# Performance work log

Measured on AMD Instinct MI355X. Metric: run time of the kernel, lower is better.

The kernel has to match this reference:

```python
import jax, jax.numpy as jnp
import numpy as np

Q_HEADS, KV_HEADS, D_K, D_V = 16, 4, 128, 128
GROUPS = Q_HEADS // KV_HEADS


def setup_inputs() -> dict:
    key = jax.random.key(0)
    ks = jax.random.split(key, 7)
    b, s, d = 2, 2048, 2048
    scale = 1.0 / np.sqrt(d).astype(np.float32)
    return {
        "Q": jax.random.normal(ks[0], (b, s, d), jnp.float32),
        "K": jax.random.normal(ks[1], (b, s, d), jnp.float32),
        "V": jax.random.normal(ks[2], (b, s, d), jnp.float32),
        "Wq": jax.random.normal(ks[3], (d, D_K * Q_HEADS), jnp.float32) * scale,
        "Wk": jax.random.normal(ks[4], (d, D_K * KV_HEADS), jnp.float32) * scale,
        "Wv": jax.random.normal(ks[5], (d, D_V * KV_HEADS), jnp.float32) * scale,
        "Wo": jax.random.normal(ks[6], (D_V * KV_HEADS, d), jnp.float32) * scale,
    }


def reference(Q, K, V, Wq, Wk, Wv, Wo):
    b, lq, _ = Q.shape
    lk = K.shape[1]
    # projections -> (b, heads, len, d)
    q = (Q @ Wq).reshape(b, lq, Q_HEADS, D_K).transpose(0, 2, 1, 3)
    k = (K @ Wk).reshape(b, lk, KV_HEADS, D_K).transpose(0, 2, 1, 3)
    v = (V @ Wv).reshape(b, lk, KV_HEADS, D_V).transpose(0, 2, 1, 3)
    # GQA quirk: scores summed over group dim g before softmax
    qr = q.reshape(b, GROUPS, KV_HEADS, lq, D_K)
    scores = jnp.einsum('bghqd,bhkd->bhqk', qr, k) / jnp.asarray(D_K ** 0.5, q.dtype)
    causal = jnp.tril(jnp.ones((lq, lk), bool))
    scores = jnp.where(causal[None, None], scores, jnp.asarray(-1e9, scores.dtype))
    attn = jax.nn.softmax(scores, axis=-1)  # (b, kv_heads, lq, lk)
    out = jnp.einsum('bhqk,bhkd->bhqd', attn, v)  # (b, kv_heads, lq, d_v)
    out = out.transpose(0, 2, 1, 3).reshape(b, lq, KV_HEADS * D_V)
    return out @ Wo
```

## Files before the change

### kernel.cpp

```cpp
#include <hip/hip_runtime.h>
#include <hip/hip_bf16.h>

typedef __attribute__((ext_vector_type(8))) short short8;
typedef __attribute__((ext_vector_type(4))) float f32x4;

#define MFMA16 __builtin_amdgcn_mfma_f32_16x16x32_bf16

__device__ inline unsigned short f2bf(float f) {
  __hip_bfloat16 h = __float2bfloat16(f);
  unsigned short u;
  __builtin_memcpy(&u, &h, 2);
  return u;
}

__device__ inline float bf2f(unsigned short u) {
  unsigned int x = ((unsigned int)u) << 16;
  float f;
  __builtin_memcpy(&f, &x, 4);
  return f;
}

__device__ inline void storeC(unsigned short* p, float v) { *p = f2bf(v); }
__device__ inline void storeC(float* p, float v) { *p = v; }

__device__ inline void gload16(const void* g, void* l) {
  __builtin_amdgcn_global_load_lds(
      (const __attribute__((address_space(1))) unsigned int*)g,
      (__attribute__((address_space(3))) unsigned int*)l,
      16, 0, 0);
}

__global__ __launch_bounds__(256)
void prep_all(const float* __restrict__ Wq, const float* __restrict__ Wk,
              const float* __restrict__ Wv, const float* __restrict__ Wo,
              unsigned short* __restrict__ Wt, unsigned short* __restrict__ WoT) {
  __shared__ float t[64][65];
  const int bid = blockIdx.x;
  const int tid = threadIdx.x;
  if (bid < 256) {
    const int n0 = (bid & 7) * 64, d0 = (bid >> 3) * 64;
#pragma unroll
    for (int it = 0; it < 16; ++it) {
      const int idx = it * 256 + tid;
      const int dd = idx >> 6, nn = idx & 63;
      const float* p = Wq + (size_t)(d0 + dd) * 2048 + n0 + nn;
      t[dd][nn] = p[0] + p[512] + p[1024] + p[1536];
    }
    __syncthreads();
#pragma unroll
    for (int it = 0; it < 16; ++it) {
      const int idx = it * 256 + tid;
      const int nn = idx >> 6, dd = idx & 63;
      Wt[(size_t)(n0 + nn) * 2048 + d0 + dd] = f2bf(t[dd][nn]);
    }
    return;
  }
  const float* src;
  unsigned short* dst;
  int R, C, c0, r0;
  if (bid < 768) {
    const int b = bid - 256;
    const int z = b >> 8;
    const int bb = b & 255;
    src = z ? Wv : Wk;
    dst = Wt + (z ? 2097152 : 1048576);
    R = 2048; C = 512;
    c0 = (bb & 7) * 64; r0 = (bb >> 3) * 64;
  } else {
    const int b = bid - 768;
    src = Wo; dst = WoT;
    R = 512; C = 2048;
    c0 = (b & 31) * 64; r0 = (b >> 5) * 64;
  }
#pragma unroll
  for (int it = 0; it < 16; ++it) {
    const int idx = it * 256 + tid;
    const int r = idx >> 6, c = idx & 63;
    t[r][c] = src[(size_t)(r0 + r) * C + c0 + c];
  }
  __syncthreads();
#pragma unroll
  for (int it = 0; it < 16; ++it) {
    const int idx = it * 256 + tid;
    const int rr = idx >> 6, cc = idx & 63;
    dst[(size_t)(c0 + rr) * R + r0 + cc] = f2bf(t[cc][rr]);
  }
}

template <bool AF32, typename CT, int KS>
__global__ __launch_bounds__(256)
void gemm_bt(const void* A0, const void* A1, const void* A2,
             const unsigned short* __restrict__ Bt, CT* __restrict__ C,
             int K, int N, size_t sB, size_t sC) {
  __shared__ unsigned short As[AF32 ? 1 : 2][128 * 64];
  __shared__ unsigned short Bs[2][128 * 64];

  const int tid = threadIdx.x;
  const int lane = tid & 63;
  const int wv = tid >> 6;
  const int wm = (wv >> 1) << 6;
  const int wn = (wv & 1) << 6;
  const int l15 = lane & 15;
  const int l4 = lane >> 4;
  const int lsw = (l15 & 7) << 4;

  const int nwg = gridDim.x;
  const int bid = blockIdx.x;
  const int job = (bid & 7) * (nwg >> 3) + (bid >> 3);
  const int ntile = N >> 7;
  const int per_ks = nwg / KS;
  const int ks = (KS > 1) ? (job / per_ks) : 0;
  const int jj = job - ks * per_ks;
  const int z = jj / (32 * ntile);
  const int rem = jj - z * 32 * ntile;
  const int m0 = (rem / ntile) << 7;
  const int n0 = (rem % ntile) << 7;
  const int kbeg = ks * (K / KS);
  const int kend = kbeg + K / KS;

  const void* Az = (z == 0) ? A0 : (z == 1) ? A1 : A2;
  const unsigned short* Ab = (const unsigned short*)Az;
  const float* Af = (const float*)Az;
  const unsigned short* Bz = Bt + sB * (size_t)z;

  const f32x4 zero = {0.f, 0.f, 0.f, 0.f};
  f32x4 acc[4][4];
#pragma unroll
  for (int i = 0; i < 4; ++i)
#pragma unroll
    for (int j = 0; j < 4; ++j) acc[i][j] = zero;

  const int srow = tid >> 3;
  const int scol = (tid & 7) << 3;
  const int scolsw = scol ^ ((srow & 7) << 3);

  float4 ar[8];

  auto issueB = [&](int buf, int k0) {
#pragma unroll
    for (int s = 0; s < 4; ++s) {
      const unsigned short* bsrc =
          Bz + (size_t)(n0 + srow + s * 32) * K + k0 + scolsw;
      gload16(bsrc, (char*)&Bs[buf][0] + tid * 16 + s * 4096);
    }
  };
  auto issueA16 = [&](int buf, int k0) {
#pragma unroll
    for (int s = 0; s < 4; ++s) {
      const unsigned short* asrc =
          Ab + (size_t)(m0 + srow + s * 32) * K + k0 + scolsw;
      gload16(asrc, (char*)&As[buf][0] + tid * 16 + s * 4096);
    }
  };
  auto loadA = [&](int k0) {
#pragma unroll
    for (int s = 0; s < 4; ++s) {
      const float* asrc = Af + (size_t)(m0 + srow + s * 32) * K + k0 + scol;
      ar[2 * s] = *(const float4*)(asrc);
      ar[2 * s + 1] = *(const float4*)(asrc + 4);
    }
  };
  auto writeA = [&]() {
#pragma unroll
    for (int s = 0; s < 4; ++s) {
      short8 o;
      o[0] = (short)f2bf(ar[2 * s].x); o[1] = (short)f2bf(ar[2 * s].y);
      o[2] = (short)f2bf(ar[2 * s].z); o[3] = (short)f2bf(ar[2 * s].w);
      o[4] = (short)f2bf(ar[2 * s + 1].x); o[5] = (short)f2bf(ar[2 * s + 1].y);
      o[6] = (short)f2bf(ar[2 * s + 1].z); o[7] = (short)f2bf(ar[2 * s + 1].w);
      *(short8*)((char*)&As[0][0] + (srow + s * 32) * 128 + scolsw * 2) = o;
    }
  };

  if constexpr (AF32) loadA(kbeg); else issueA16(0, kbeg);
  issueB(0, kbeg);

  int cur = 0;
  for (int k0 = kbeg; k0 < kend; k0 += 64) {
    const bool more = (k0 + 64 < kend);
    asm volatile("s_waitcnt vmcnt(0)" ::: "memory");
    if constexpr (AF32) {
      writeA();
      if (more) { issueB(cur ^ 1, k0 + 64); loadA(k0 + 64); }
      asm volatile("s_waitcnt lgkmcnt(0)" ::: "memory");
    } else {
      if (more) { issueA16(cur ^ 1, k0 + 64); issueB(cur ^ 1, k0 + 64); }
    }
    __builtin_amdgcn_s_barrier();
    const unsigned short* as = AF32 ? &As[0][0] : &As[cur][0];
#pragma unroll
    for (int kk = 0; kk < 2; ++kk) {
      const int kb = (kk * 64 + (l4 << 4)) ^ lsw;
      short8 a[4], b[4];
#pragma unroll
      for (int i = 0; i < 4; ++i)
        a[i] = *(const short8*)((const char*)as + (wm + i * 16 + l15) * 128 + kb);
#pragma unroll
      for (int j = 0; j < 4; ++j)
        b[j] = *(const short8*)((const char*)&Bs[cur][0] +
                                (wn + j * 16 + l15) * 128 + kb);
#pragma unroll
      for (int i = 0; i < 4; ++i)
#pragma unroll
        for (int j = 0; j < 4; ++j)
          acc[i][j] = MFMA16(a[i], b[j], acc[i][j], 0, 0, 0);
    }
    __builtin_amdgcn_s_barrier();
    cur ^= 1;
  }

  CT* Cz = C + sC * (size_t)(ks * 3 + z);
#pragma unroll
  for (int i = 0; i < 4; ++i) {
    const int row0 = m0 + wm + i * 16 + (l4 << 2);
#pragma unroll
    for (int j = 0; j < 4; ++j) {
      const int col = n0 + wn + j * 16 + l15;
#pragma unroll
      for (int r = 0; r < 4; ++r)
        storeC(&Cz[(size_t)(row0 + r) * N + col], acc[i][j][r]);
    }
  }
}

__global__ __launch_bounds__(256)
void qkv_pack(const unsigned short* __restrict__ pC,
              unsigned short* __restrict__ qpack,
              unsigned short* __restrict__ kpack) {
  const size_t SLOTE = 6291456;
  const int idx = blockIdx.x * 256 + threadIdx.x;
  const int lane = idx & 63;
  const int kk = (idx >> 6) & 3;
  const int qb = (idx >> 8) & 127;
  const int bh = idx >> 15;
  const int row = (bh >> 2) * 2048 + qb * 16 + (lane & 15);
  const int col = (bh & 3) * 128 + kk * 32 + (lane >> 4) * 8;
  const size_t off = (size_t)row * 512 + col;
  {
    const short8 a = *(const short8*)(pC + off);
    const short8 b = *(const short8*)(pC + SLOTE + off);
    short8 o;
#pragma unroll
    for (int e = 0; e < 8; ++e)
      o[e] = (short)f2bf(bf2f((unsigned short)a[e]) + bf2f((unsigned short)b[e]));
    *(short8*)(qpack + (size_t)idx * 8) = o;
  }
  {
    const short8 a = *(const short8*)(pC + 2097152 + off);
    const short8 b = *(const short8*)(pC + SLOTE + 2097152 + off);
    short8 o;
#pragma unroll
    for (int e = 0; e < 8; ++e)
      o[e] = (short)f2bf(bf2f((unsigned short)a[e]) + bf2f((unsigned short)b[e]));
    *(short8*)(kpack + (size_t)idx * 8) = o;
  }
}

__global__ __launch_bounds__(256)
void vpack_k(const unsigned short* __restrict__ pC,
             unsigned short* __restrict__ vpack) {
  __shared__ unsigned short t[32][132];
  const int kvb = blockIdx.x;
  const int bh = blockIdx.y;
  const int brow = (bh >> 2) * 2048;
  const int h = bh & 3;
  const int tid = threadIdx.x;
  const unsigned short* v0 = pC + 4194304;
  const unsigned short* v1 = pC + 6291456 + 4194304;
#pragma unroll
  for (int it = 0; it < 2; ++it) {
    const int idx = it * 256 + tid;
    const int r = idx >> 4;
    const int c8 = (idx & 15) << 3;
    const size_t off = (size_t)(brow + kvb * 32 + r) * 512 + h * 128 + c8;
    const short8 xa = *(const short8*)(v0 + off);
    const short8 xb = *(const short8*)(v1 + off);
    short8 o;
#pragma unroll
    for (int e = 0; e < 8; ++e)
      o[e] = (short)f2bf(bf2f((unsigned short)xa[e]) + bf2f((unsigned short)xb[e]));
    *(short8*)&t[r][c8] = o;
  }
  __syncthreads();
#pragma unroll
  for (int it = 0; it < 2; ++it) {
    const int idx = it * 256 + tid;
    const int d8 = idx >> 6;
    const int lane = idx & 63;
    const int l15 = lane & 15;
    const int l4 = lane >> 4;
    short8 o;
#pragma unroll
    for (int e = 0; e < 8; ++e) o[e] = (short)t[l4 * 8 + e][d8 * 16 + l15];
    *(short8*)(vpack + ((((size_t)bh * 64 + kvb) * 8 + d8) * 64 + lane) * 8) = o;
  }
}

__global__ __launch_bounds__(128, 1)
void attn_split(const unsigned short* __restrict__ qpack,
                const unsigned short* __restrict__ kpack,
                const unsigned short* __restrict__ vpack,
                unsigned short* __restrict__ Oh,
                unsigned short* __restrict__ pO,
                float* __restrict__ pml) {
  __shared__ unsigned short P_lds[2][32][36];
  const int tid = threadIdx.x;
  const int lane = tid & 63;
  const int wave = tid >> 6;
  const int l15 = lane & 15;
  const int l4 = lane >> 4;
  const int bh = blockIdx.x & 7;
  const int jid = 143 - (int)(blockIdx.x >> 3);
  const int brow = (bh >> 2) * 2048;
  const int h = bh & 3;

  int j = jid, g = 0;
  while (j >= 2 * (g + 1) * (g + 2)) ++g;
  const int rem = j - 2 * g * (g + 1);
  const int r_ = rem / (g + 1);
  const int c_ = rem - r_ * (g + 1);
  const int qt = 4 * g + r_;
  const int k_begin = c_ << 8;
  const int k_end = (c_ == g) ? (qt + 1) * 64 : ((c_ + 1) << 8);
  const int qrow_w = qt * 64 + wave * 32;
  const float SCALE2 = 0.127517424f;

  short8 qf[2][4];
#pragma unroll
  for (int m = 0; m < 2; ++m)
#pragma unroll
    for (int kk = 0; kk < 4; ++kk)
      qf[m][kk] = *(const short8*)(qpack +
          ((((size_t)bh * 128 + (qrow_w >> 4) + m) * 4 + kk) * 64 + lane) * 8);

  short8 oneb;
#pragma unroll
  for (int e = 0; e < 8; ++e) oneb[e] = (short)0x3F80;

  const f32x4 zero = {0.f, 0.f, 0.f, 0.f};
  f32x4 o_acc[2][8];
  f32x4 l_acc[2];
#pragma unroll
  for (int m = 0; m < 2; ++m) {
    l_acc[m] = zero;
#pragma unroll
    for (int i = 0; i < 8; ++i) o_acc[m][i] = zero;
  }

  const int nt = (k_end - k_begin) >> 5;
  int ntv = ((qrow_w + 31 - k_begin) >> 5) + 1;
  if (ntv > nt) ntv = nt;

  auto loadK = [&](short8 (&kf)[2][4], int t) {
    const int kvb = (k_begin >> 4) + t * 2;
#pragma unroll
    for (int n = 0; n < 2; ++n)
#pragma unroll
      for (int kk = 0; kk < 4; ++kk)
        kf[n][kk] = *(const short8*)(kpack +
            ((((size_t)bh * 128 + kvb + n) * 4 + kk) * 64 + lane) * 8);
  };
  auto loadV = [&](short8 (&vb)[8], int t) {
    const int kvb32 = (k_begin >> 5) + t;
#pragma unroll
    for (int d8 = 0; d8 < 8; ++d8)
      vb[d8] = *(const short8*)(vpack +
          ((((size_t)bh * 64 + kvb32) * 8 + d8) * 64 + lane) * 8);
  };
  auto compute = [&](int t, short8 (&kf)[2][4], short8 (&vb)[8]) {
    const int kbase = k_begin + t * 32;
    f32x4 sa[2][2];
    sa[0][0] = zero; sa[0][1] = zero; sa[1][0] = zero; sa[1][1] = zero;
#pragma unroll
    for (int n = 0; n < 2; ++n)
#pragma unroll
      for (int kk = 0; kk < 4; ++kk) {
        sa[0][n] = MFMA16(qf[0][kk], kf[n][kk], sa[0][n], 0, 0, 0);
        sa[1][n] = MFMA16(qf[1][kk], kf[n][kk], sa[1][n], 0, 0, 0);
      }
    const bool need_mask = (kbase + 31 > qrow_w);
    float p[2][2][4];
#pragma unroll
    for (int m = 0; m < 2; ++m)
#pragma unroll
      for (int n = 0; n < 2; ++n)
#pragma unroll
        for (int r = 0; r < 4; ++r) {
          const float v = exp2f(sa[m][n][r] * SCALE2 - 24.f);
          bool msk = false;
          if (need_mask) {
            const int kc = kbase + n * 16 + l15;
            const int qr = qrow_w + m * 16 + (l4 << 2) + r;
            msk = (kc > qr);
          }
          p[m][n][r] = msk ? 0.f : v;
        }
#pragma unroll
    for (int m = 0; m < 2; ++m)
#pragma unroll
      for (int n = 0; n < 2; ++n)
#pragma unroll
        for (int r = 0; r < 4; ++r)
          P_lds[wave][m * 16 + (l4 << 2) + r][n * 16 + l15] = f2bf(p[m][n][r]);
    short8 pa[2];
#pragma unroll
    for (int m = 0; m < 2; ++m)
      pa[m] = *(const short8*)((const char*)&P_lds[wave][0][0] +
                               (m * 16 + l15) * 72 + (l4 << 4));
    l_acc[0] = MFMA16(pa[0], oneb, l_acc[0], 0, 0, 0);
    l_acc[1] = MFMA16(pa[1], oneb, l_acc[1], 0, 0, 0);
#pragma unroll
    for (int d8 = 0; d8 < 8; ++d8) {
      o_acc[0][d8] = MFMA16(pa[0], vb[d8], o_acc[0][d8], 0, 0, 0);
      o_acc[1][d8] = MFMA16(pa[1], vb[d8], o_acc[1][d8], 0, 0, 0);
    }
  };

  short8 kfA[2][4], vbA[8], kfB[2][4], vbB[8];
  loadK(kfA, 0);
  loadV(vbA, 0);
  for (int t = 0; t < ntv; t += 2) {
    if (t + 1 < ntv) { loadK(kfB, t + 1); loadV(vbB, t + 1); }
    compute(t, kfA, vbA);
    if (t + 1 < ntv) {
      if (t + 2 < ntv) { loadK(kfA, t + 2); loadV(vbA, t + 2); }
      compute(t + 1, kfB, vbB);
    }
  }

  if (g == 0) {
#pragma unroll
    for (int m = 0; m < 2; ++m)
#pragma unroll
      for (int d8 = 0; d8 < 8; ++d8)
#pragma unroll
        for (int r = 0; r < 4; ++r) {
          const int row = brow + qrow_w + m * 16 + (l4 << 2) + r;
          Oh[(size_t)row * 512 + h * 128 + d8 * 16 + l15] =
              f2bf(o_acc[m][d8][r] / l_acc[m][r]);
        }
  } else {
    const int slot = bh * 144 + jid;
    unsigned short* po = pO + (size_t)slot * 64 * 128;
#pragma unroll
    for (int m = 0; m < 2; ++m)
#pragma unroll
      for (int d8 = 0; d8 < 8; ++d8)
#pragma unroll
        for (int r = 0; r < 4; ++r) {
          const int row = wave * 32 + m * 16 + (l4 << 2) + r;
          po[row * 128 + d8 * 16 + l15] = f2bf(o_acc[m][d8][r]);
        }
    if (l15 == 0) {
#pragma unroll
      for (int m = 0; m < 2; ++m)
#pragma unroll
        for (int r = 0; r < 4; ++r) {
          const int row = wave * 32 + m * 16 + (l4 << 2) + r;
          pml[((size_t)slot * 64 + row) * 2 + 0] = 0.f;
          pml[((size_t)slot * 64 + row) * 2 + 1] = l_acc[m][r];
        }
    }
  }
}

__global__ __launch_bounds__(256)
void attn_combine(const unsigned short* __restrict__ pO,
                  const float* __restrict__ pml,
                  unsigned short* __restrict__ Oh) {
  const int bh = blockIdx.y;
  const int qt = 4 + blockIdx.x;
  const int g = qt >> 2;
  const int nch = g + 1;
  const int base = 2 * g * (g + 1) + (qt & 3) * (g + 1);
  const int slot0 = bh * 144 + base;
  const int brow = (bh >> 2) * 2048;
  const int h = bh & 3;
#pragma unroll
  for (int u = 0; u < 4; ++u) {
    const int unit = u * 256 + threadIdx.x;
    const int row = unit >> 4;
    const int c8 = (unit & 15) << 3;
    float M = -1e30f;
    for (int c = 0; c < nch; ++c)
      M = fmaxf(M, pml[((size_t)(slot0 + c) * 64 + row) * 2]);
    float L = 0.f;
    float acc[8] = {0.f, 0.f, 0.f, 0.f, 0.f, 0.f, 0.f, 0.f};
    for (int c = 0; c < nch; ++c) {
      const float mc = pml[((size_t)(slot0 + c) * 64 + row) * 2];
      const float lc = pml[((size_t)(slot0 + c) * 64 + row) * 2 + 1];
      const float w = exp2f(mc - M);
      L += w * lc;
      const short8 ov =
          *(const short8*)(pO + ((size_t)(slot0 + c) * 64 + row) * 128 + c8);
#pragma unroll
      for (int e = 0; e < 8; ++e) acc[e] += w * bf2f((unsigned short)ov[e]);
    }
    const float inv = 1.f / L;
    short8 o;
#pragma unroll
    for (int e = 0; e < 8; ++e) o[e] = (short)f2bf(acc[e] * inv);
    *(short8*)(Oh + (size_t)(brow + qt * 64 + row) * 512 + h * 128 + c8) = o;
  }
}

extern "C" void kernel_launch(void* const* d_in, const int* in_sizes, int n_in,
                              void* d_out, int out_size, void* d_ws, size_t ws_size,
                              hipStream_t stream) {
  const float* Q  = (const float*)d_in[0];
  const float* K_ = (const float*)d_in[1];
  const float* V  = (const float*)d_in[2];
  const float* Wq = (const float*)d_in[3];
  const float* Wk = (const float*)d_in[4];
  const float* Wv = (const float*)d_in[5];
  const float* Wo = (const float*)d_in[6];
  float* out = (float*)d_out;

  char* ws = (char*)d_ws;
  unsigned short* Wt    = (unsigned short*)ws;
  unsigned short* WoT   = (unsigned short*)(ws + 6291456);
  unsigned short* qpack = (unsigned short*)(ws + 8388608);
  unsigned short* kpack = (unsigned short*)(ws + 12582912);
  unsigned short* vpack = (unsigned short*)(ws + 16777216);
  unsigned short* Oh    = (unsigned short*)(ws + 20971520);
  unsigned short* pC    = (unsigned short*)(ws + 20971520);
  unsigned short* pO    = (unsigned short*)(ws + 25165824);
  float*          pml   = (float*)(ws + 48234496);

  prep_all<<<1024, 256, 0, stream>>>(Wq, Wk, Wv, Wo, Wt, WoT);

  gemm_bt<true, unsigned short, 2><<<768, 256, 0, stream>>>(
      Q, K_, V, Wt, pC, 2048, 512, 1048576, 2097152);
  qkv_pack<<<1024, 256, 0, stream>>>(pC, qpack, kpack);
  vpack_k<<<dim3(64, 8), 256, 0, stream>>>(pC, vpack);

  attn_split<<<1152, 128, 0, stream>>>(qpack, kpack, vpack, Oh, pO, pml);
  attn_combine<<<dim3(28, 8), 256, 0, stream>>>(pO, pml, Oh);

  gemm_bt<false, float, 1><<<512, 256, 0, stream>>>(
      Oh, Oh, Oh, WoT, out, 512, 2048, 0, 0);
}
```

Before: 127.1 us.

## Pre-convert inputs to bf16 and use 3-stage pipelined GEMM without split-K

Adds a separate kernel that converts Q, K and V from fp32 to bf16 up front. Replaces the dual-path GEMM with a single bf16 GEMM that uses a 3-buffer LDS pipeline with BK=32, direct global-to-LDS loads, an XOR swizzle, setprio around the MFMAs, and occupancy 2. Drops split-K in the projection GEMM, so the pack kernels become plain copies with no partial-sum reduction. The cost is an extra pass over 48M fp32 values and fewer workgroups (384) for the projection GEMM.

```diff
diff --git a/kernel.cpp b/kernel.cpp
--- a/kernel.cpp
+++ b/kernel.cpp
@@ -87,13 +87,32 @@
   }
 }
 
-template <bool AF32, typename CT, int KS>
 __global__ __launch_bounds__(256)
-void gemm_bt(const void* A0, const void* A1, const void* A2,
-             const unsigned short* __restrict__ Bt, CT* __restrict__ C,
-             int K, int N, size_t sB, size_t sC) {
-  __shared__ unsigned short As[AF32 ? 1 : 2][128 * 64];
-  __shared__ unsigned short Bs[2][128 * 64];
+void conv_bf16(const float* __restrict__ Q, const float* __restrict__ K_,
+               const float* __restrict__ V, unsigned short* __restrict__ dst) {
+  const int z = blockIdx.y;
+  const float* src = (z == 0) ? Q : (z == 1) ? K_ : V;
+  unsigned short* d = dst + (size_t)z * 8388608;
+  size_t i = ((size_t)blockIdx.x * 256 + threadIdx.x) * 8;
+  const size_t stride = (size_t)gridDim.x * 256 * 8;
+  for (; i < 8388608; i += stride) {
+    const float4 v0 = *(const float4*)(src + i);
+    const float4 v1 = *(const float4*)(src + i + 4);
+    short8 o;
+    o[0] = (short)f2bf(v0.x); o[1] = (short)f2bf(v0.y);
+    o[2] = (short)f2bf(v0.z); o[3] = (short)f2bf(v0.w);
+    o[4] = (short)f2bf(v1.x); o[5] = (short)f2bf(v1.y);
+    o[6] = (short)f2bf(v1.z); o[7] = (short)f2bf(v1.w);
+    *(short8*)(d + i) = o;
+  }
+}
+
+template <typename CT>
+__global__ __launch_bounds__(256, 2)
+void gemm3t(const unsigned short* __restrict__ A,
+            const unsigned short* __restrict__ Bt, CT* __restrict__ C,
+            int K, int N, int ntile, size_t sA, size_t sB, size_t sC) {
+  __shared__ char lds[49152];
 
   const int tid = threadIdx.x;
   const int lane = tid & 63;
@@ -102,25 +121,16 @@
   const int wn = (wv & 1) << 6;
   const int l15 = lane & 15;
   const int l4 = lane >> 4;
-  const int lsw = (l15 & 7) << 4;
 
   const int nwg = gridDim.x;
   const int bid = blockIdx.x;
   const int job = (bid & 7) * (nwg >> 3) + (bid >> 3);
-  const int ntile = N >> 7;
-  const int per_ks = nwg / KS;
-  const int ks = (KS > 1) ? (job / per_ks) : 0;
-  const int jj = job - ks * per_ks;
-  const int z = jj / (32 * ntile);
-  const int rem = jj - z * 32 * ntile;
+  const int z = job / (32 * ntile);
+  const int rem = job - z * 32 * ntile;
   const int m0 = (rem / ntile) << 7;
   const int n0 = (rem % ntile) << 7;
-  const int kbeg = ks * (K / KS);
-  const int kend = kbeg + K / KS;
-
-  const void* Az = (z == 0) ? A0 : (z == 1) ? A1 : A2;
-  const unsigned short* Ab = (const unsigned short*)Az;
-  const float* Af = (const float*)Az;
+
+  const unsigned short* Az = A + sA * (size_t)z;
   const unsigned short* Bz = Bt + sB * (size_t)z;
 
   const f32x4 zero = {0.f, 0.f, 0.f, 0.f};
@@ -130,86 +140,71 @@
 #pragma unroll
     for (int j = 0; j < 4; ++j) acc[i][j] = zero;
 
-  const int srow = tid >> 3;
-  const int scol = (tid & 7) << 3;
-  const int scolsw = scol ^ ((srow & 7) << 3);
-
-  float4 ar[8];
-
-  auto issueB = [&](int buf, int k0) {
-#pragma unroll
-    for (int s = 0; s < 4; ++s) {
-      const unsigned short* bsrc =
-          Bz + (size_t)(n0 + srow + s * 32) * K + k0 + scolsw;
-      gload16(bsrc, (char*)&Bs[buf][0] + tid * 16 + s * 4096);
+  auto stage = [&](int buf, int k0) {
+#pragma unroll
+    for (int i = 0; i < 2; ++i) {
+      const int flat = i * 4096 + tid * 16;
+      const int r = flat >> 6;
+      const int colb = (flat & 63) ^ ((r & 3) << 4);
+      gload16((const char*)(Az + (size_t)(m0 + r) * K + k0) + colb,
+              lds + buf * 16384 + flat);
+    }
+#pragma unroll
+    for (int i = 0; i < 2; ++i) {
+      const int flat = i * 4096 + tid * 16;
+      const int r = flat >> 6;
+      const int colb = (flat & 63) ^ ((r & 3) << 4);
+      gload16((const char*)(Bz + (size_t)(n0 + r) * K + k0) + colb,
+              lds + buf * 16384 + 8192 + flat);
     }
   };
-  auto issueA16 = [&](int buf, int k0) {
-#pragma unroll
-    for (int s = 0; s < 4; ++s) {
-      const unsigned short* asrc =
-          Ab + (size_t)(m0 + srow + s * 32) * K + k0 + scolsw;
-      gload16(asrc, (char*)&As[buf][0] + tid * 16 + s * 4096);
-    }
-  };
-  auto loadA = [&](int k0) {
-#pragma unroll
-    for (int s = 0; s < 4; ++s) {
-      const float* asrc = Af + (size_t)(m0 + srow + s * 32) * K + k0 + scol;
-      ar[2 * s] = *(const float4*)(asrc);
-      ar[2 * s + 1] = *(const float4*)(asrc + 4);
-    }
-  };
-  auto writeA = [&]() {
-#pragma unroll
-    for (int s = 0; s < 4; ++s) {
-      short8 o;
-      o[0] = (short)f2bf(ar[2 * s].x); o[1] = (short)f2bf(ar[2 * s].y);
-      o[2] = (short)f2bf(ar[2 * s].z); o[3] = (short)f2bf(ar[2 * s].w);
-      o[4] = (short)f2bf(ar[2 * s + 1].x); o[5] = (short)f2bf(ar[2 * s + 1].y);
-      o[6] = (short)f2bf(ar[2 * s + 1].z); o[7] = (short)f2bf(ar[2 * s + 1].w);
-      *(short8*)((char*)&As[0][0] + (srow + s * 32) * 128 + scolsw * 2) = o;
-    }
-  };
-
-  if constexpr (AF32) loadA(kbeg); else issueA16(0, kbeg);
-  issueB(0, kbeg);
-
-  int cur = 0;
-  for (int k0 = kbeg; k0 < kend; k0 += 64) {
-    const bool more = (k0 + 64 < kend);
-    asm volatile("s_waitcnt vmcnt(0)" ::: "memory");
-    if constexpr (AF32) {
-      writeA();
-      if (more) { issueB(cur ^ 1, k0 + 64); loadA(k0 + 64); }
-      asm volatile("s_waitcnt lgkmcnt(0)" ::: "memory");
-    } else {
-      if (more) { issueA16(cur ^ 1, k0 + 64); issueB(cur ^ 1, k0 + 64); }
-    }
-    __builtin_amdgcn_s_barrier();
-    const unsigned short* as = AF32 ? &As[0][0] : &As[cur][0];
-#pragma unroll
-    for (int kk = 0; kk < 2; ++kk) {
-      const int kb = (kk * 64 + (l4 << 4)) ^ lsw;
-      short8 a[4], b[4];
-#pragma unroll
-      for (int i = 0; i < 4; ++i)
-        a[i] = *(const short8*)((const char*)as + (wm + i * 16 + l15) * 128 + kb);
+
+  const int NS = K >> 5;
+
+  stage(0, 0);
+  stage(1, 32);
+  asm volatile("s_waitcnt vmcnt(4)" ::: "memory");
+  __builtin_amdgcn_sched_barrier(0);
+  __builtin_amdgcn_s_barrier();
+  __builtin_amdgcn_sched_barrier(0);
+
+  int b = 0;
+  for (int s = 0; s < NS; ++s) {
+    const int b2 = (b + 2 >= 3) ? (b - 1) : (b + 2);
+    if (s + 2 < NS) stage(b2, (s + 2) << 5);
+    const char* L = lds + b * 16384;
+    short8 a[4], bf[4];
+#pragma unroll
+    for (int i = 0; i < 4; ++i) {
+      const int r = wm + i * 16 + l15;
+      a[i] = *(const short8*)(L + r * 64 + ((l4 << 4) ^ ((r & 3) << 4)));
+    }
+#pragma unroll
+    for (int j = 0; j < 4; ++j) {
+      const int r = wn + j * 16 + l15;
+      bf[j] = *(const short8*)(L + 8192 + r * 64 + ((l4 << 4) ^ ((r & 3) << 4)));
+    }
+    __builtin_amdgcn_s_setprio(1);
+#pragma unroll
+    for (int i = 0; i < 4; ++i)
 #pragma unroll
       for (int j = 0; j < 4; ++j)
-        b[j] = *(const short8*)((const char*)&Bs[cur][0] +
-                                (wn + j * 16 + l15) * 128 + kb);
-#pragma unroll
-      for (int i = 0; i < 4; ++i)
-#pragma unroll
-        for (int j = 0; j < 4; ++j)
-          acc[i][j] = MFMA16(a[i], b[j], acc[i][j], 0, 0, 0);
-    }
-    __builtin_amdgcn_s_barrier();
-    cur ^= 1;
-  }
-
-  CT* Cz = C + sC * (size_t)(ks * 3 + z);
+        acc[i][j] = MFMA16(a[i], bf[j], acc[i][j], 0, 0, 0);
+    __builtin_amdgcn_s_setprio(0);
+    if (s + 1 < NS) {
+      if (s + 2 < NS) {
+        asm volatile("s_waitcnt vmcnt(4)" ::: "memory");
+      } else {
+        asm volatile("s_waitcnt vmcnt(0)" ::: "memory");
+      }
+      __builtin_amdgcn_sched_barrier(0);
+      __builtin_amdgcn_s_barrier();
+      __builtin_amdgcn_sched_barrier(0);
+    }
+    b = (b + 1 == 3) ? 0 : b + 1;
+  }
+
+  CT* Cz = C + sC * (size_t)z;
 #pragma unroll
   for (int i = 0; i < 4; ++i) {
     const int row0 = m0 + wm + i * 16 + (l4 << 2);
@@ -224,10 +219,10 @@
 }
 
 __global__ __launch_bounds__(256)
-void qkv_pack(const unsigned short* __restrict__ pC,
+void qkv_pack(const unsigned short* __restrict__ qh,
+              const unsigned short* __restrict__ kh,
               unsigned short* __restrict__ qpack,
               unsigned short* __restrict__ kpack) {
-  const size_t SLOTE = 6291456;
   const int idx = blockIdx.x * 256 + threadIdx.x;
   const int lane = idx & 63;
   const int kk = (idx >> 6) & 3;
@@ -236,28 +231,12 @@
   const int row = (bh >> 2) * 2048 + qb * 16 + (lane & 15);
   const int col = (bh & 3) * 128 + kk * 32 + (lane >> 4) * 8;
   const size_t off = (size_t)row * 512 + col;
-  {
-    const short8 a = *(const short8*)(pC + off);
-    const short8 b = *(const short8*)(pC + SLOTE + off);
-    short8 o;
-#pragma unroll
-    for (int e = 0; e < 8; ++e)
-      o[e] = (short)f2bf(bf2f((unsigned short)a[e]) + bf2f((unsigned short)b[e]));
-    *(short8*)(qpack + (size_t)idx * 8) = o;
-  }
-  {
-    const short8 a = *(const short8*)(pC + 2097152 + off);
-    const short8 b = *(const short8*)(pC + SLOTE + 2097152 + off);
-    short8 o;
-#pragma unroll
-    for (int e = 0; e < 8; ++e)
-      o[e] = (short)f2bf(bf2f((unsigned short)a[e]) + bf2f((unsigned short)b[e]));
-    *(short8*)(kpack + (size_t)idx * 8) = o;
-  }
+  *(short8*)(qpack + (size_t)idx * 8) = *(const short8*)(qh + off);
+  *(short8*)(kpack + (size_t)idx * 8) = *(const short8*)(kh + off);
 }
 
 __global__ __launch_bounds__(256)
-void vpack_k(const unsigned short* __restrict__ pC,
+void vpack_k(const unsigned short* __restrict__ vh,
              unsigned short* __restrict__ vpack) {
   __shared__ unsigned short t[32][132];
   const int kvb = blockIdx.x;
@@ -265,21 +244,13 @@
   const int brow = (bh >> 2) * 2048;
   const int h = bh & 3;
   const int tid = threadIdx.x;
-  const unsigned short* v0 = pC + 4194304;
-  const unsigned short* v1 = pC + 6291456 + 4194304;
 #pragma unroll
   for (int it = 0; it < 2; ++it) {
     const int idx = it * 256 + tid;
     const int r = idx >> 4;
     const int c8 = (idx & 15) << 3;
     const size_t off = (size_t)(brow + kvb * 32 + r) * 512 + h * 128 + c8;
-    const short8 xa = *(const short8*)(v0 + off);
-    const short8 xb = *(const short8*)(v1 + off);
-    short8 o;
-#pragma unroll
-    for (int e = 0; e < 8; ++e)
-      o[e] = (short)f2bf(bf2f((unsigned short)xa[e]) + bf2f((unsigned short)xb[e]));
-    *(short8*)&t[r][c8] = o;
+    *(short8*)&t[r][c8] = *(const short8*)(vh + off);
   }
   __syncthreads();
 #pragma unroll
@@ -519,24 +490,31 @@
   char* ws = (char*)d_ws;
   unsigned short* Wt    = (unsigned short*)ws;
   unsigned short* WoT   = (unsigned short*)(ws + 6291456);
+  unsigned short* Abf   = (unsigned short*)(ws + 8388608);
+  unsigned short* qh    = (unsigned short*)(ws + 33554432);
+  unsigned short* kh    = (unsigned short*)(ws + 37748736);
+  unsigned short* vh    = (unsigned short*)(ws + 41943040);
   unsigned short* qpack = (unsigned short*)(ws + 8388608);
   unsigned short* kpack = (unsigned short*)(ws + 12582912);
   unsigned short* vpack = (unsigned short*)(ws + 16777216);
   unsigned short* Oh    = (unsigned short*)(ws + 20971520);
-  unsigned short* pC    = (unsigned short*)(ws + 20971520);
   unsigned short* pO    = (unsigned short*)(ws + 25165824);
   float*          pml   = (float*)(ws + 48234496);
 
   prep_all<<<1024, 256, 0, stream>>>(Wq, Wk, Wv, Wo, Wt, WoT);
-
-  gemm_bt<true, unsigned short, 2><<<768, 256, 0, stream>>>(
-      Q, K_, V, Wt, pC, 2048, 512, 1048576, 2097152);
-  qkv_pack<<<1024, 256, 0, stream>>>(pC, qpack, kpack);
-  vpack_k<<<dim3(64, 8), 256, 0, stream>>>(pC, vpack);
+  conv_bf16<<<dim3(1024, 3), 256, 0, stream>>>(Q, K_, V, Abf);
+
+  gemm3t<unsigned short><<<384, 256, 0, stream>>>(
+      Abf, Wt, qh, 2048, 512, 4,
+      8388608, 1048576, 2097152);
+
+  qkv_pack<<<1024, 256, 0, stream>>>(qh, kh, qpack, kpack);
+  vpack_k<<<dim3(64, 8), 256, 0, stream>>>(vh, vpack);
 
   attn_split<<<1152, 128, 0, stream>>>(qpack, kpack, vpack, Oh, pO, pml);
   attn_combine<<<dim3(28, 8), 256, 0, stream>>>(pO, pml, Oh);
 
-  gemm_bt<false, float, 1><<<512, 256, 0, stream>>>(
-      Oh, Oh, Oh, WoT, out, 512, 2048, 0, 0);
-}
+  gemm3t<float><<<512, 256, 0, stream>>>(
+      Oh, WoT, out, 512, 2048, 16,
+      0, 0, 0);
+}
```

Measured after the change: 151.8 us. +19.5%, slower.
